# Kernel optimization log

Hardware: AMD Instinct MI355X
Metric: run time of the kernel (lower is better)

## Reference

```python
import jax, jax.numpy as jnp
import numpy as np

B, T, D = 2, 2048, 2048
H, HD = 16, 128          # n_heads, head_dim = d_out // n_heads
DC, DR = 512, 64         # latent dim d_c, rope dim d_R


def _rope(x):
    """RoPE over last dim (even), positions along axis -2. x: [..., T, Dr]."""
    half = x.shape[-1] // 2
    t = x.shape[-2]
    inv_freq = 1.0 / (10000.0 ** (jnp.arange(half, dtype=jnp.float32) / half))
    freqs = jnp.arange(t, dtype=jnp.float32)[:, None] * inv_freq[None, :]  # [T, half]
    sin, cos = jnp.sin(freqs), jnp.cos(freqs)
    x1, x2 = x[..., :half], x[..., half:]
    # stack pairs on a new last axis then flatten -> interleaved layout,
    # matching torch.stack((...), dim=-1) followed by implicit flatten
    rot = jnp.stack([x1 * cos - x2 * sin, x1 * sin + x2 * cos], axis=-1)
    return rot.reshape(x.shape[:-1] + (2 * half,))


def setup_inputs() -> dict:
    key = jax.random.key(0)
    ks = jax.random.split(key, 10)
    s = 0.02  # init scale
    return {
        "x":     jax.random.normal(ks[0], (B, T, D), dtype=jnp.float32),
        "W_DKV": jax.random.normal(ks[1], (D, DC), dtype=jnp.float32) * s,
        "W_DQ":  jax.random.normal(ks[2], (D, DC), dtype=jnp.float32) * s,
        "W_UK":  jax.random.normal(ks[3], (DC, D), dtype=jnp.float32) * s,
        "W_UV":  jax.random.normal(ks[4], (DC, D), dtype=jnp.float32) * s,
        "W_UQ":  jax.random.normal(ks[5], (DC, D), dtype=jnp.float32) * s,
        "W_KR":  jax.random.normal(ks[6], (D, DR), dtype=jnp.float32) * s,
        "W_QR":  jax.random.normal(ks[7], (DC, H * DR), dtype=jnp.float32) * s,
        "W_O":   jax.random.normal(ks[8], (D, D), dtype=jnp.float32) * s,
        "b_O":   jax.random.normal(ks[9], (D,), dtype=jnp.float32) * s,
    }


def reference(x, W_DKV, W_DQ, W_UK, W_UV, W_UQ, W_KR, W_QR, W_O, b_O):
    b, t, d = x.shape
    # latent KV compression and up-projection
    c_kv = x @ W_DKV                                        # [B,T,d_c]
    K = (c_kv @ W_UK).reshape(b, t, H, HD).transpose(0, 2, 1, 3)  # [B,H,T,hd]
    V = (c_kv @ W_UV).reshape(b, t, H, HD).transpose(0, 2, 1, 3)
    # latent Q compression and up-projection
    c_q = x @ W_DQ                                          # [B,T,d_c]
    Q = (c_q @ W_UQ).reshape(b, t, H, HD).transpose(0, 2, 1, 3)
    # decoupled RoPE channels: shared rotary key per token, per-head rotary query
    k_R = _rope(x @ W_KR)[:, None, :, :]                    # [B,1,T,d_R]
    k_R = jnp.broadcast_to(k_R, (b, H, t, DR))
    q_R = (c_q @ W_QR).reshape(b, t, H, DR).transpose(0, 2, 1, 3)  # [B,H,T,d_R]
    q_R = _rope(q_R)
    # concat content + rotary channels
    Kf = jnp.concatenate([K, k_R], axis=-1)                 # [B,H,T,hd+d_R]
    Qf = jnp.concatenate([Q, q_R], axis=-1)
    scale = 1.0 / jnp.sqrt(jnp.float32(HD + DR))
    scores = jnp.einsum('bhqd,bhkd->bhqk', Qf, Kf) * scale  # [B,H,T,T]
    attn = jax.nn.softmax(scores, axis=-1)                  # dropout is identity (p=0 / eval)
    ctx = jnp.einsum('bhqk,bhkd->bhqd', attn, V)            # [B,H,T,hd]
    ctx = ctx.transpose(0, 2, 1, 3).reshape(b, t, d)
    return ctx @ W_O + b_O
```

## Files before the change

### kernel.cpp

```cpp
#include <hip/hip_runtime.h>
#include <hip/hip_bf16.h>

typedef __attribute__((ext_vector_type(8))) short short8;
typedef __attribute__((ext_vector_type(4))) short s4_t;
typedef __attribute__((ext_vector_type(4))) float f32x4;
typedef __attribute__((ext_vector_type(16))) float f32x16;
typedef __attribute__((ext_vector_type(2))) unsigned uint2v;
typedef __hip_bfloat16 bf16;

#define NB 2
#define NT 2048
#define NDIM 2048
#define NH 16
#define NHD 128
#define NDC 512
#define NDR 64

__device__ __forceinline__ void gl_lds16(const bf16* g, bf16* l){
  __builtin_amdgcn_global_load_lds(
      (const __attribute__((address_space(1))) void*)(const void*)g,
      (__attribute__((address_space(3))) void*)(void*)l, 16, 0, 0);
}

__global__ __launch_bounds__(256) void cvt_kernel(const float* __restrict__ src, bf16* __restrict__ dst){
  int i = (blockIdx.x*256 + threadIdx.x)*4;
  float4 v = *(const float4*)(src + i);
  dst[i+0] = __float2bfloat16(v.x);
  dst[i+1] = __float2bfloat16(v.y);
  dst[i+2] = __float2bfloat16(v.z);
  dst[i+3] = __float2bfloat16(v.w);
}

struct TAll {
  const float* src[8];
  bf16* dst[8];
  int K[8];
  int N[8];
  int cum[9];
};
__global__ __launch_bounds__(256) void tconv_all(TAll a){
  __shared__ float tile[32][33];
  int bid = blockIdx.x;
  int i = 0;
  #pragma unroll
  for (int j=0;j<8;j++) if (bid >= a.cum[j+1]) i = j+1;
  const float* W = a.src[i];
  bf16* Wt = a.dst[i];
  int K = a.K[i], N = a.N[i];
  int tl = bid - a.cum[i];
  int ntx = N >> 5;
  int n0 = (tl % ntx)*32, k0 = (tl / ntx)*32;
  int tx = threadIdx.x & 31, ty = threadIdx.x >> 5;
  #pragma unroll
  for (int j=0;j<32;j+=8) tile[ty+j][tx] = W[(size_t)(k0+ty+j)*N + n0 + tx];
  __syncthreads();
  #pragma unroll
  for (int j=0;j<32;j+=8) Wt[(size_t)(n0+ty+j)*K + k0 + tx] = __float2bfloat16(tile[tx][ty+j]);
}

template<int MODE>
__global__ __launch_bounds__(256,3) void gemm_bt(const bf16* __restrict__ A,
    const bf16* __restrict__ Bt, bf16* __restrict__ C, bf16* __restrict__ C2,
    float* __restrict__ Cf, const float* __restrict__ bias,
    int M, int N, int K, int lda, float mult)
{
  __shared__ bf16 As[128*64];
  __shared__ bf16 Bs[128*64];
  const int m0 = blockIdx.x*128, n0 = blockIdx.y*128;
  const int t = threadIdx.x, lane = t&63, w = t>>6;
  const int wr = w>>1, wc = w&1;
  const int l15 = lane&15, lg = lane>>4;
  const int wbase = t & 192;

  f32x4 acc[4][4];
  #pragma unroll
  for (int mi=0;mi<4;mi++)
    #pragma unroll
    for (int nj=0;nj<4;nj++) acc[mi][nj] = (f32x4){0.f,0.f,0.f,0.f};

  for (int k0=0;k0<K;k0+=64){
    __syncthreads();
    #pragma unroll
    for (int j=0;j<4;j++){
      int c = j*256 + t;
      int r = c>>3, cc = (c&7)*8;
      gl_lds16(A + (size_t)(m0+r)*lda + k0 + cc, As + (size_t)(j*256 + wbase)*8);
      int bn = n0 + r; if (bn > N-1) bn = N-1;
      gl_lds16(Bt + (size_t)bn*K + k0 + cc, Bs + (size_t)(j*256 + wbase)*8);
    }
    __syncthreads();
    #pragma unroll
    for (int kk=0;kk<2;kk++){
      short8 af[4], bfv[4];
      #pragma unroll
      for (int mi=0;mi<4;mi++) af[mi] = *(const short8*)&As[(wr*64+mi*16+l15)*64 + kk*32+lg*8];
      #pragma unroll
      for (int nj=0;nj<4;nj++) bfv[nj] = *(const short8*)&Bs[(wc*64+nj*16+l15)*64 + kk*32+lg*8];
      #pragma unroll
      for (int mi=0;mi<4;mi++)
        #pragma unroll
        for (int nj=0;nj<4;nj++)
          acc[mi][nj] = __builtin_amdgcn_mfma_f32_16x16x32_bf16(af[mi], bfv[nj], acc[mi][nj], 0,0,0);
    }
  }

  #pragma unroll
  for (int mi=0;mi<4;mi++){
    #pragma unroll
    for (int nj=0;nj<4;nj++){
      f32x4 v = acc[mi][nj];
      int gr0 = m0 + wr*64 + mi*16 + lg*4;
      int gc  = n0 + wc*64 + nj*16 + l15;
      if constexpr (MODE==0){
        if (gc < N){
          #pragma unroll
          for (int r2=0;r2<4;r2++) C[(size_t)(gr0+r2)*N + gc] = __float2bfloat16(v[r2]*mult);
        }
      } else if constexpr (MODE==2){
        float bb = bias[gc];
        #pragma unroll
        for (int r2=0;r2<4;r2++) Cf[(size_t)(gr0+r2)*N + gc] = v[r2]*mult + bb;
      } else if constexpr (MODE==4){
        int bidx = m0 >> 11;
        int tl0 = (m0 & 2047) + wr*64 + mi*16 + lg*4;
        if (gc < 2048){
          int hq = gc >> 7, dl = gc & 127;
          size_t base = ((size_t)bidx*NH + hq)*(size_t)NT;
          #pragma unroll
          for (int r2=0;r2<4;r2++) C[(base + tl0 + r2)*192 + dl] = __float2bfloat16(v[r2]);
        } else {
          int g2 = gc - 2048;
          int hq = g2 >> 7, dl = g2 & 127;
          s4_t pk;
          #pragma unroll
          for (int r2=0;r2<4;r2++){
            union { bf16 b; unsigned short u; } cvu;
            cvu.b = __float2bfloat16(v[r2]);
            pk[r2] = (short)cvu.u;
          }
          *(s4_t*)&C2[(((size_t)bidx*NH + hq)*NHD + dl)*NT + tl0] = pk;
        }
      } else {
        if (gc < 2048){
          int bidx = m0 >> 11;
          int tl0 = (m0 & 2047) + wr*64 + mi*16 + lg*4;
          int hq = gc >> 7, dl = gc & 127;
          size_t base = ((size_t)bidx*NH + hq)*(size_t)NT;
          #pragma unroll
          for (int r2=0;r2<4;r2++) C[(base + tl0 + r2)*192 + dl] = __float2bfloat16(v[r2]*mult);
        } else {
          #pragma unroll
          for (int r2=0;r2<4;r2++) C2[(size_t)(gr0+r2)*1024 + (gc-2048)] = __float2bfloat16(v[r2]);
        }
      }
    }
  }
}

__global__ __launch_bounds__(128) void rope_kernel(const bf16* __restrict__ krp,
    const bf16* __restrict__ qrp, bf16* __restrict__ Kf, bf16* __restrict__ Qf)
{
  int bt = blockIdx.x*2 + (threadIdx.x>>6);
  int d = threadIdx.x & 63;
  int b = bt >> 11, tpos = bt & 2047;
  int i = d >> 1;
  const float scale = 0.07216878364870323f;
  float inv = __expf(-(float)i * 0.2878231366242557f);
  float fr = (float)tpos * inv;
  float sn, cs;
  sincosf(fr, &sn, &cs);

  float x1 = __bfloat162float(krp[(size_t)bt*1088 + i]);
  float x2 = __bfloat162float(krp[(size_t)bt*1088 + 32 + i]);
  float kv = (d&1) ? (x1*sn + x2*cs) : (x1*cs - x2*sn);
  bf16 kvb = __float2bfloat16(kv);
  size_t base = ((size_t)b*NH*NT + tpos)*192;
  #pragma unroll
  for (int h=0;h<NH;h++) Kf[base + (size_t)h*NT*192 + 128 + d] = kvb;

  #pragma unroll
  for (int h=0;h<NH;h++){
    float y1 = __bfloat162float(qrp[bt*1024 + h*64 + i]);
    float y2 = __bfloat162float(qrp[bt*1024 + h*64 + 32 + i]);
    float qv = (d&1) ? (y1*sn + y2*cs) : (y1*cs - y2*sn);
    Qf[base + (size_t)h*NT*192 + 128 + d] = __float2bfloat16(qv*scale);
  }
}

static __device__ inline void plswap(unsigned &a, unsigned &b){
  uint2v r = __builtin_amdgcn_permlane32_swap(a, b, false, false);
  a = r[0]; b = r[1];
}
static __device__ inline unsigned cvtpk(float lo, float hi){
  unsigned u;
  asm("v_cvt_pk_bf16_f32 %0, %1, %2" : "=v"(u) : "v"(lo), "v"(hi));
  return u;
}

__global__ __launch_bounds__(256,2) void attn_kernel(const bf16* __restrict__ Qf,
    const bf16* __restrict__ Kf, const bf16* __restrict__ Vt, bf16* __restrict__ ctx)
{
  __shared__ __align__(16) char smem[81920];

  const int lin = blockIdx.x;
  const int swz = (lin & 7)*64 + (lin >> 3);
  const int qt = swz & 15, bh = swz >> 4;
  const int b = bh >> 4, h = bh & 15;
  const int q0 = qt * 128;
  const int t = threadIdx.x, lane = t&63, w = t>>6;
  const int l31 = lane&31, hi = lane>>5;
  const int rsw = (l31&7)<<4;
  const int hib = hi*16;

  const bf16* Qp  = Qf + ((size_t)bh*NT + q0)*192;
  const bf16* Kp  = Kf + (size_t)bh*NT*192;
  const bf16* Vtp = Vt + (size_t)bh*NHD*NT;

  short8 qf[12];
  #pragma unroll
  for (int kk=0;kk<12;kk++)
    qf[kk] = *(const short8*)(Qp + (size_t)(w*32 + l31)*192 + kk*16 + hi*8);

  f32x16 o[4];
  #pragma unroll
  for (int Dt=0;Dt<4;Dt++)
    #pragma unroll
    for (int r=0;r<16;r++) o[Dt][r] = 0.f;
  float mrun = -1e30f, lrun = 0.f;

  short8 kst[6], vst[4];
  auto load_tile = [&](int kt){
    const bf16* Ksrc = Kp + (size_t)kt*64*192;
    #pragma unroll
    for (int j=0;j<6;j++) kst[j] = *(const short8*)(Ksrc + (j*256+t)*8);
    #pragma unroll
    for (int j=0;j<4;j++){
      int c = j*256 + t;
      vst[j] = *(const short8*)(Vtp + (size_t)(c>>3)*NT + kt*64 + (c&7)*8);
    }
  };
  load_tile(0);

  for (int kt=0; kt<NT/64; kt++){
    char* KsB  = smem + (kt&1)*40960;
    char* VTsB = KsB + 24576;
    #pragma unroll
    for (int j=0;j<6;j++){
      int c = j*256 + t;
      int r = c/24, cb = (c%24)*16;
      *(short8*)(KsB + r*384 + (cb ^ ((r&7)<<4))) = kst[j];
    }
    #pragma unroll
    for (int j=0;j<4;j++){
      int c = j*256 + t;
      int r = c>>3, cb = (c&7)*16;
      *(short8*)(VTsB + r*128 + (cb ^ ((r&7)<<4))) = vst[j];
    }
    if (kt+1 < NT/64) load_tile(kt+1);
    __syncthreads();

    f32x16 sa[2];
    #pragma unroll
    for (int Mt=0;Mt<2;Mt++)
      #pragma unroll
      for (int r=0;r<16;r++) sa[Mt][r] = 0.f;
    __builtin_amdgcn_s_setprio(1);
    #pragma unroll
    for (int kk=0;kk<12;kk++){
      int cb = kk*32 + hib;
      short8 kf0 = *(const short8*)(KsB + (size_t)l31*384        + ((cb) ^ rsw));
      short8 kf1 = *(const short8*)(KsB + (size_t)(l31+32)*384   + ((cb) ^ rsw));
      sa[0] = __builtin_amdgcn_mfma_f32_32x32x16_bf16(kf0, qf[kk], sa[0], 0,0,0);
      sa[1] = __builtin_amdgcn_mfma_f32_32x32x16_bf16(kf1, qf[kk], sa[1], 0,0,0);
    }
    __builtin_amdgcn_s_setprio(0);

    float mx[8];
    #pragma unroll
    for (int i2=0;i2<8;i2++)
      mx[i2] = fmaxf(fmaxf(sa[0][2*i2], sa[0][2*i2+1]), fmaxf(sa[1][2*i2], sa[1][2*i2+1]));
    float tm = fmaxf(fmaxf(fmaxf(mx[0],mx[1]),fmaxf(mx[2],mx[3])),
                     fmaxf(fmaxf(mx[4],mx[5]),fmaxf(mx[6],mx[7])));
    tm = fmaxf(tm, __shfl_xor(tm, 32));

    if (__any(tm > mrun + 8.f)){
      float mn = fmaxf(mrun, tm);
      float alpha = __expf(mrun - mn);
      mrun = mn;
      lrun *= alpha;
      #pragma unroll
      for (int Dt=0;Dt<4;Dt++)
        #pragma unroll
        for (int r=0;r<16;r++) o[Dt][r] *= alpha;
    }

    #pragma unroll
    for (int Mt=0;Mt<2;Mt++)
      #pragma unroll
      for (int r=0;r<16;r++) sa[Mt][r] = __expf(sa[Mt][r] - mrun);
    float sm[8];
    #pragma unroll
    for (int i2=0;i2<8;i2++)
      sm[i2] = (sa[0][2*i2] + sa[0][2*i2+1]) + (sa[1][2*i2] + sa[1][2*i2+1]);
    float rs = ((sm[0]+sm[1])+(sm[2]+sm[3])) + ((sm[4]+sm[5])+(sm[6]+sm[7]));
    rs += __shfl_xor(rs, 32);
    lrun += rs;

    short8 pf[4];
    #pragma unroll
    for (int Mt=0;Mt<2;Mt++){
      unsigned u[8];
      #pragma unroll
      for (int p8=0;p8<8;p8++) u[p8] = cvtpk(sa[Mt][2*p8], sa[Mt][2*p8+1]);
      plswap(u[0], u[2]); plswap(u[1], u[3]);
      plswap(u[4], u[6]); plswap(u[5], u[7]);
      union { unsigned du[4]; short8 s8; } f0, f1;
      f0.du[0]=u[0]; f0.du[1]=u[1]; f0.du[2]=u[2]; f0.du[3]=u[3];
      f1.du[0]=u[4]; f1.du[1]=u[5]; f1.du[2]=u[6]; f1.du[3]=u[7];
      pf[2*Mt+0] = f0.s8;
      pf[2*Mt+1] = f1.s8;
    }

    __builtin_amdgcn_s_setprio(1);
    #pragma unroll
    for (int kw=0;kw<4;kw++){
      int cb = kw*32 + hib;
      #pragma unroll
      for (int Dt=0;Dt<4;Dt++){
        short8 vf = *(const short8*)(VTsB + (size_t)(Dt*32 + l31)*128 + ((cb) ^ rsw));
        o[Dt] = __builtin_amdgcn_mfma_f32_32x32x16_bf16(vf, pf[kw], o[Dt], 0,0,0);
      }
    }
    __builtin_amdgcn_s_setprio(0);
  }

  __syncthreads();
  float il = 1.0f / lrun;
  bf16* Es = (bf16*)smem;
  const int EROW = 136;
  const int ebase = w*32*EROW;
  #pragma unroll
  for (int Dt=0;Dt<4;Dt++)
    #pragma unroll
    for (int r=0;r<16;r++){
      int d = Dt*32 + (r&3) + 8*(r>>2) + 4*hi;
      Es[ebase + l31*EROW + d] = __float2bfloat16(o[Dt][r]*il);
    }
  __syncthreads();
  int q = lane>>1, halfd = lane&1;
  size_t gq = q0 + w*32 + q;
  size_t obase = (((size_t)b*NT + gq)*NH + h)*NHD + halfd*64;
  #pragma unroll
  for (int pp=0;pp<8;pp++)
    *(short8*)&ctx[obase + pp*8] = *(short8*)&Es[ebase + q*EROW + halfd*64 + pp*8];
}

extern "C" void kernel_launch(void* const* d_in, const int* in_sizes, int n_in,
                              void* d_out, int out_size, void* d_ws, size_t ws_size,
                              hipStream_t stream)
{
  const float* x     = (const float*)d_in[0];
  const float* W_DKV = (const float*)d_in[1];
  const float* W_DQ  = (const float*)d_in[2];
  const float* W_UK  = (const float*)d_in[3];
  const float* W_UV  = (const float*)d_in[4];
  const float* W_UQ  = (const float*)d_in[5];
  const float* W_KR  = (const float*)d_in[6];
  const float* W_QR  = (const float*)d_in[7];
  const float* W_O   = (const float*)d_in[8];
  const float* b_O   = (const float*)d_in[9];

  const float scale = 0.07216878364870323f;

  char* ws = (char*)d_ws;
  bf16* xb    = (bf16*)(ws + 0);
  bf16* wcomb = (bf16*)(ws + 16777216);
  bf16* wuk   = (bf16*)(ws + 21233664);
  bf16* wuv   = (bf16*)(ws + 23330816);
  bf16* wuq   = (bf16*)(ws + 25427968);
  bf16* wqr   = (bf16*)(ws + 27525120);
  bf16* wo    = (bf16*)(ws + 28573696);
  bf16* comb  = (bf16*)(ws + 36962304);
  bf16* qrp   = (bf16*)(ws + 45875200);
  bf16* Qf    = (bf16*)(ws + 54263808);
  bf16* Kf    = (bf16*)(ws + 79429632);
  bf16* vt    = (bf16*)(ws + 104595456);
  bf16* ctxb  = (bf16*)(ws + 121372672);

  bf16* ckv = comb;
  bf16* cq  = comb + 512;
  bf16* krp = comb + 1024;

  cvt_kernel<<<8192,256,0,stream>>>(x, xb);

  TAll ta;
  ta.src[0]=W_DKV; ta.dst[0]=wcomb;             ta.K[0]=2048; ta.N[0]=512;
  ta.src[1]=W_DQ;  ta.dst[1]=wcomb + 512*2048;  ta.K[1]=2048; ta.N[1]=512;
  ta.src[2]=W_KR;  ta.dst[2]=wcomb + 1024*2048; ta.K[2]=2048; ta.N[2]=64;
  ta.src[3]=W_UK;  ta.dst[3]=wuk;               ta.K[3]=512;  ta.N[3]=2048;
  ta.src[4]=W_UV;  ta.dst[4]=wuv;               ta.K[4]=512;  ta.N[4]=2048;
  ta.src[5]=W_UQ;  ta.dst[5]=wuq;               ta.K[5]=512;  ta.N[5]=2048;
  ta.src[6]=W_QR;  ta.dst[6]=wqr;               ta.K[6]=512;  ta.N[6]=1024;
  ta.src[7]=W_O;   ta.dst[7]=wo;                ta.K[7]=2048; ta.N[7]=2048;
  ta.cum[0]=0;
  for (int i=0;i<8;i++) ta.cum[i+1] = ta.cum[i] + (ta.N[i]/32)*(ta.K[i]/32);
  tconv_all<<<ta.cum[8],256,0,stream>>>(ta);

  gemm_bt<0><<<dim3(32,9), 256,0,stream>>>(xb, wcomb, comb, nullptr, nullptr, nullptr, 4096, 1088, 2048, 2048, 1.0f);

  gemm_bt<4><<<dim3(32,32),256,0,stream>>>(ckv, wuk, Kf, vt, nullptr, nullptr, 4096, 4096, 512, 1088, 1.0f);
  gemm_bt<5><<<dim3(32,24),256,0,stream>>>(cq, wuq, Qf, qrp, nullptr, nullptr, 4096, 3072, 512, 1088, scale);

  rope_kernel<<<2048,128,0,stream>>>(krp, qrp, Kf, Qf);
  attn_kernel<<<512,256,0,stream>>>(Qf, Kf, vt, ctxb);
  gemm_bt<2><<<dim3(32,16),256,0,stream>>>(ctxb, wo, nullptr, nullptr, (float*)d_out, b_O, 4096, 2048, 2048, 2048, 1.0f);
}
```

Baseline: 272.3 us.

## Pre-swizzle V layout in projection and load V fragments directly from global

The projection epilogue now writes V in a fragment-ordered layout, with each 64-token tile split into kw/hi sub-blocks of 128 dims by 8 tokens. The attention kernel can then load V MFMA operands straight from global memory into registers, skipping LDS staging. Shared memory drops to K double buffering only (48KB), which cuts LDS traffic and raises the occupancy headroom. The cost is extra registers for 16 V fragments per tile and global-load latency, which is only partly hidden by issuing half of them before the QK MFMAs.

```diff
diff --git a/kernel.cpp b/kernel.cpp
--- a/kernel.cpp
+++ b/kernel.cpp
@@ -131,6 +131,7 @@
         } else {
           int g2 = gc - 2048;
           int hq = g2 >> 7, dl = g2 & 127;
+          int kt = tl0 >> 6, kw = (tl0>>4)&3, hi2 = (tl0>>3)&1, j0 = tl0&7;
           s4_t pk;
           #pragma unroll
           for (int r2=0;r2<4;r2++){
@@ -138,7 +139,8 @@
             cvu.b = __float2bfloat16(v[r2]);
             pk[r2] = (short)cvu.u;
           }
-          *(s4_t*)&C2[(((size_t)bidx*NH + hq)*NHD + dl)*NT + tl0] = pk;
+          size_t base = (((size_t)(bidx*NH + hq)*32 + kt)*8 + kw*2 + hi2)*1024 + dl*8 + j0;
+          *(s4_t*)&C2[base] = pk;
         }
       } else {
         if (gc < 2048){
@@ -200,7 +202,7 @@
 __global__ __launch_bounds__(256,2) void attn_kernel(const bf16* __restrict__ Qf,
     const bf16* __restrict__ Kf, const bf16* __restrict__ Vt, bf16* __restrict__ ctx)
 {
-  __shared__ __align__(16) char smem[81920];
+  __shared__ __align__(16) char smem[49152];
 
   const int lin = blockIdx.x;
   const int swz = (lin & 7)*64 + (lin >> 3);
@@ -228,35 +230,30 @@
     for (int r=0;r<16;r++) o[Dt][r] = 0.f;
   float mrun = -1e30f, lrun = 0.f;
 
-  short8 kst[6], vst[4];
-  auto load_tile = [&](int kt){
+  short8 kst[6];
+  auto load_k = [&](int kt){
     const bf16* Ksrc = Kp + (size_t)kt*64*192;
     #pragma unroll
     for (int j=0;j<6;j++) kst[j] = *(const short8*)(Ksrc + (j*256+t)*8);
-    #pragma unroll
-    for (int j=0;j<4;j++){
-      int c = j*256 + t;
-      vst[j] = *(const short8*)(Vtp + (size_t)(c>>3)*NT + kt*64 + (c&7)*8);
-    }
   };
-  load_tile(0);
+  load_k(0);
 
   for (int kt=0; kt<NT/64; kt++){
-    char* KsB  = smem + (kt&1)*40960;
-    char* VTsB = KsB + 24576;
+    char* KsB = smem + (kt&1)*24576;
     #pragma unroll
     for (int j=0;j<6;j++){
       int c = j*256 + t;
       int r = c/24, cb = (c%24)*16;
       *(short8*)(KsB + r*384 + (cb ^ ((r&7)<<4))) = kst[j];
     }
-    #pragma unroll
-    for (int j=0;j<4;j++){
-      int c = j*256 + t;
-      int r = c>>3, cb = (c&7)*16;
-      *(short8*)(VTsB + r*128 + (cb ^ ((r&7)<<4))) = vst[j];
-    }
-    if (kt+1 < NT/64) load_tile(kt+1);
+    const bf16* Vb2 = Vtp + (size_t)kt*8192;
+    short8 vA[8], vB[8];
+    #pragma unroll
+    for (int kw=0;kw<2;kw++)
+      #pragma unroll
+      for (int Dt=0;Dt<4;Dt++)
+        vA[kw*4+Dt] = *(const short8*)(Vb2 + (kw*2+hi)*1024 + (Dt*32+l31)*8);
+    if (kt+1 < NT/64) load_k(kt+1);
     __syncthreads();
 
     f32x16 sa[2];
@@ -274,6 +271,12 @@
       sa[1] = __builtin_amdgcn_mfma_f32_32x32x16_bf16(kf1, qf[kk], sa[1], 0,0,0);
     }
     __builtin_amdgcn_s_setprio(0);
+
+    #pragma unroll
+    for (int kw=0;kw<2;kw++)
+      #pragma unroll
+      for (int Dt=0;Dt<4;Dt++)
+        vB[kw*4+Dt] = *(const short8*)(Vb2 + ((kw+2)*2+hi)*1024 + (Dt*32+l31)*8);
 
     float mx[8];
     #pragma unroll
@@ -324,10 +327,9 @@
     __builtin_amdgcn_s_setprio(1);
     #pragma unroll
     for (int kw=0;kw<4;kw++){
-      int cb = kw*32 + hib;
       #pragma unroll
       for (int Dt=0;Dt<4;Dt++){
-        short8 vf = *(const short8*)(VTsB + (size_t)(Dt*32 + l31)*128 + ((cb) ^ rsw));
+        short8 vf = (kw<2) ? vA[kw*4+Dt] : vB[(kw-2)*4+Dt];
         o[Dt] = __builtin_amdgcn_mfma_f32_32x32x16_bf16(vf, pf[kw], o[Dt], 0,0,0);
       }
     }
```

New measurement: 299.4 us. 1.1x slower.
